# Performance work log

Measured on AMD Instinct MI355X. Metric: run time of the kernel, lower is better.

## Reference

```python
import jax, jax.numpy as jnp
import numpy as np

DIM = 1024

def setup_inputs() -> dict:
    key = jax.random.key(0)
    k1, k2, k3, k4 = jax.random.split(key, 4)
    B, L, D = 32, 2048, DIM
    x = jax.random.normal(k1, (B, D), dtype=jnp.float32)
    context = jax.random.normal(k2, (B, L, D), dtype=jnp.float32)
    # linear_concatWa: Linear(2*dim, dim, bias=False) -> weight [dim, 2*dim]
    Wa = jax.random.normal(k3, (D, 2 * D), dtype=jnp.float32) * (1.0 / np.sqrt(2 * D))
    # linear_concatVa: Linear(dim, 1, bias=False) -> weight [1, dim]
    Va = jax.random.normal(k4, (1, D), dtype=jnp.float32) * (1.0 / np.sqrt(D))
    return {"x": x, "context": context, "Wa": Wa, "Va": Va}


def reference(x, context, Wa, Va):
    # concat-mode additive (Bahdanau) attention.
    # Wa @ cat(ht, hs) == ht @ Wa[:, :D].T + hs @ Wa[:, D:].T  (avoids materializing concat)
    D = x.shape[-1]
    Wa_t, Wa_s = Wa[:, :D], Wa[:, D:]              # each [D, D]
    ht_proj = jnp.einsum('bd,kd->bk', x, Wa_t)     # [B, D]
    hs_proj = jnp.einsum('bld,kd->blk', context, Wa_s)  # [B, L, D]
    hidden = jnp.tanh(ht_proj[:, None, :] + hs_proj)    # [B, L, D]
    scores = jnp.einsum('blk,ok->bl', hidden, Va)       # [B, L]  (Va: [1, D])
    attn = jax.nn.softmax(scores, axis=-1)               # [B, L]
    weighted = jnp.einsum('bl,bld->bd', attn, context)   # [B, D]
    return weighted, attn
```

## Files before the change

kernel.cpp:

```cpp
#include <hip/hip_runtime.h>
#include <hip/hip_bf16.h>
#include <cstdint>
#include <cstddef>

#define DIM 1024
#define B_SZ 32
#define L_SZ 2048

#define BM 128
#define BN 128

#define CVT_BLOCKS 8192
#define HT_BLOCKS  512
#define WA_BLOCKS  512

typedef __attribute__((ext_vector_type(8))) short bf16x8;
typedef __attribute__((ext_vector_type(4))) float floatx4;

static __device__ __forceinline__ unsigned cvt2_bf16_rne(float a, float b) {
    unsigned ua = __builtin_bit_cast(unsigned, a);
    unsigned ub = __builtin_bit_cast(unsigned, b);
    ua = (ua + 0x7FFFu + ((ua >> 16) & 1u)) >> 16;
    ub = (ub + 0x7FFFu + ((ub >> 16) & 1u)) >> 16;
    return ua | (ub << 16);
}

static __device__ __forceinline__ float bf2f(unsigned u16) {
    return __builtin_bit_cast(float, u16 << 16);
}

static __device__ __forceinline__ float tanh_fast(float x) {
    float e = __expf(2.0f * x);
    return 1.0f - 2.0f * __builtin_amdgcn_rcpf(e + 1.0f);
}

static __device__ __forceinline__ void gld_lds16(const void* g, void* lds) {
    __builtin_amdgcn_global_load_lds(
        (const __attribute__((address_space(1))) unsigned int*)g,
        (__attribute__((address_space(3))) unsigned int*)lds,
        16, 0, 0);
}

static __device__ __forceinline__ bf16x8 dsr128(unsigned addr) {
    bf16x8 r;
    asm volatile("ds_read_b128 %0, %1" : "=v"(r) : "v"(addr));
    return r;
}

#define VMCNT(n)  asm volatile("s_waitcnt vmcnt(" #n ")" ::: "memory")
#define SBAR()    asm volatile("s_barrier" ::: "memory")
#define WAITK()   do { asm volatile("s_waitcnt lgkmcnt(0)" ::: "memory"); \
                       __builtin_amdgcn_sched_barrier(0); } while (0)

__global__ __launch_bounds__(256) void pre_kernel(
    const float* __restrict__ x, const float* __restrict__ ctx,
    const float* __restrict__ Wa,
    unsigned short* __restrict__ ctxB, unsigned short* __restrict__ WaB,
    float* __restrict__ ht, float* __restrict__ scores,
    float* __restrict__ weighted)
{
    const int bid = blockIdx.x, t = threadIdx.x;

    if (bid < CVT_BLOCKS) {
        const long n8 = (long)B_SZ * L_SZ * DIM / 8;
        const long stride = (long)CVT_BLOCKS * 256;
        for (long i = (long)bid * 256 + t; i < n8; i += stride) {
            const float4 a = ((const float4*)ctx)[i * 2];
            const float4 b = ((const float4*)ctx)[i * 2 + 1];
            uint4 o;
            o.x = cvt2_bf16_rne(a.x, a.y);
            o.y = cvt2_bf16_rne(a.z, a.w);
            o.z = cvt2_bf16_rne(b.x, b.y);
            o.w = cvt2_bf16_rne(b.z, b.w);
            ((uint4*)ctxB)[i] = o;
        }
    } else if (bid < CVT_BLOCKS + HT_BLOCKS) {
        const int lb = bid - CVT_BLOCKS;
        const int gi = lb * 256 + t;
        if (gi < B_SZ * L_SZ) scores[gi] = 0.f;
        const int b = lb >> 4, kb = lb & 15;
        __shared__ float xs[DIM];
        for (int i = t; i < DIM; i += 256) xs[i] = x[b * DIM + i];
        __syncthreads();
        const int wave = t >> 6, lane = t & 63;
        const float4* xs4 = (const float4*)xs;
        for (int kk = 0; kk < 16; ++kk) {
            const int k = kb * 64 + wave * 16 + kk;
            const float4* wr = (const float4*)(Wa + (size_t)k * (2 * DIM));
            float s = 0.f;
            #pragma unroll
            for (int d = 0; d < DIM / 4; d += 64) {
                const float4 w4 = wr[d + lane];
                const float4 x4 = xs4[d + lane];
                s += w4.x * x4.x + w4.y * x4.y + w4.z * x4.z + w4.w * x4.w;
            }
            #pragma unroll
            for (int off = 32; off > 0; off >>= 1) s += __shfl_xor(s, off);
            if (lane == 0) ht[b * DIM + k] = s;
        }
    } else {
        const int lb = bid - CVT_BLOCKS - HT_BLOCKS;
        const int i = lb * 256 + t;
        if (i < B_SZ * DIM) weighted[i] = 0.f;
        const int k = i >> 7, dc = i & 127;
        const float* s = Wa + (size_t)k * (2 * DIM) + DIM + dc * 8;
        const float4 a = ((const float4*)s)[0];
        const float4 b4 = ((const float4*)s)[1];
        uint4 o;
        o.x = cvt2_bf16_rne(a.x, a.y);
        o.y = cvt2_bf16_rne(a.z, a.w);
        o.z = cvt2_bf16_rne(b4.x, b4.y);
        o.w = cvt2_bf16_rne(b4.z, b4.w);
        ((uint4*)(WaB + (size_t)k * DIM + dc * 8))[0] = o;
    }
}

static __device__ __forceinline__ void lda4(
    unsigned base, int wr, int l15, int quad, bf16x8 (&af)[4][2])
{
    #pragma unroll
    for (int i = 0; i < 4; ++i) {
        const int r = wr + i * 16 + l15;
        #pragma unroll
        for (int kb = 0; kb < 2; ++kb) {
            const int c = (kb * 4 + quad) ^ (r & 7);
            af[i][kb] = dsr128(base + (unsigned)(r * 128 + c * 16));
        }
    }
}

static __device__ __forceinline__ void ldb2(
    unsigned base, int wc, int l15, int quad, bf16x8 (&bv)[2][2])
{
    #pragma unroll
    for (int j = 0; j < 2; ++j) {
        const int r = wc + j * 16 + l15;
        #pragma unroll
        for (int kb = 0; kb < 2; ++kb) {
            const int c = (kb * 4 + quad) ^ (r & 7);
            bv[j][kb] = dsr128(base + (unsigned)(r * 128 + c * 16));
        }
    }
}

static __device__ __forceinline__ void mma16(
    floatx4 (&acc)[4][2], const bf16x8 (&af)[4][2], const bf16x8 (&bv)[2][2])
{
    __builtin_amdgcn_s_setprio(1);
    #pragma unroll
    for (int kb = 0; kb < 2; ++kb)
        #pragma unroll
        for (int i = 0; i < 4; ++i)
            #pragma unroll
            for (int j = 0; j < 2; ++j)
                acc[i][j] = __builtin_amdgcn_mfma_f32_16x16x32_bf16(
                    af[i][kb], bv[j][kb], acc[i][j], 0, 0, 0);
    __builtin_amdgcn_s_setprio(0);
}

static __device__ __forceinline__ void stage_half(
    const unsigned short* __restrict__ g, unsigned short* lds, int t, int wave)
{
    #pragma unroll
    for (int q = 0; q < 2; ++q) {
        const int ch = q * 512 + t;
        const int lr = ch >> 3;
        const int lc = (ch & 7) ^ (lr & 7);
        gld_lds16(g + (size_t)lr * DIM + lc * 8, lds + (q * 512 + wave * 64) * 8);
    }
}

__global__ __launch_bounds__(512, 2) void gemm_score_8ph(
    const unsigned short* __restrict__ A, const unsigned short* __restrict__ Bm,
    const float* __restrict__ Va, const float* __restrict__ ht,
    float* __restrict__ scores)
{
    __shared__ __align__(16) unsigned short As[2][2][128 * 64];
    __shared__ __align__(16) unsigned short Bs[2][2][128 * 64];

    const int bid = blockIdx.x;
    const int logical = (bid & 7) * 128 + (bid >> 3);
    const int m0 = (logical >> 2) * 256;
    const int n0 = (logical & 3) * 256;

    const int t = threadIdx.x;
    const int lane = t & 63, wave = t >> 6;
    const int l15 = lane & 15, quad = lane >> 4;
    const int wr = (wave >> 2) * 64;
    const int wc = (wave & 3) * 32;

    const unsigned short* Ag = A + (size_t)m0 * DIM;
    const unsigned short* Bg = Bm + (size_t)n0 * DIM;

    const unsigned aB = (unsigned)(unsigned long long)&As[0][0][0];
    const unsigned bB = (unsigned)(unsigned long long)&Bs[0][0][0];
    const unsigned a00 = aB, a01 = aB + 16384, a10 = aB + 32768, a11 = aB + 49152;
    const unsigned b00 = bB, b01 = bB + 16384, b10 = bB + 32768, b11 = bB + 49152;

    floatx4 acc[4][4][2];
    #pragma unroll
    for (int q = 0; q < 4; ++q)
        #pragma unroll
        for (int i = 0; i < 4; ++i)
            #pragma unroll
            for (int j = 0; j < 2; ++j) acc[q][i][j] = (floatx4)0.f;

    bf16x8 af[4][2], bvA[2][2], bvB[2][2];

    stage_half(Ag, &As[0][0][0], t, wave);
    stage_half(Bg, &Bs[0][0][0], t, wave);
    stage_half(Bg + (size_t)128 * DIM, &Bs[0][1][0], t, wave);
    stage_half(Ag + (size_t)128 * DIM, &As[0][1][0], t, wave);
    stage_half(Ag + 64, &As[1][0][0], t, wave);
    stage_half(Bg + (size_t)128 * DIM + 64, &Bs[1][1][0], t, wave);
    VMCNT(4);
    SBAR();

    for (int it = 0; it < 8; ++it) {
        const int k1 = (2 * it + 1) * 64;
        const int k2 = (2 * it + 2) * 64;
        const int k3 = (2 * it + 3) * 64;
        const bool more = (it < 7);

        lda4(a00, wr, l15, quad, af);
        ldb2(b00, wc, l15, quad, bvA);
        stage_half(Bg + k1, &Bs[1][0][0], t, wave);
        SBAR();
        WAITK();
        mma16(acc[0], af, bvA);
        SBAR();

        ldb2(b01, wc, l15, quad, bvB);
        stage_half(Ag + (size_t)128 * DIM + k1, &As[1][1][0], t, wave);
        if (more) stage_half(Bg + k2, &Bs[0][0][0], t, wave);
        SBAR();
        WAITK();
        mma16(acc[1], af, bvB);
        SBAR();

        lda4(a01, wr, l15, quad, af);
        SBAR();
        WAITK();
        mma16(acc[3], af, bvB);
        SBAR();

        if (more) { stage_half(Ag + k2, &As[0][0][0], t, wave); VMCNT(2); }
        else      { VMCNT(0); }
        SBAR();
        mma16(acc[2], af, bvA);
        SBAR();

        lda4(a10, wr, l15, quad, af);
        ldb2(b10, wc, l15, quad, bvA);
        if (more) stage_half(Bg + (size_t)128 * DIM + k2, &Bs[0][1][0], t, wave);
        SBAR();
        WAITK();
        mma16(acc[0], af, bvA);
        SBAR();

        ldb2(b11, wc, l15, quad, bvB);
        if (more) stage_half(Ag + (size_t)128 * DIM + k2, &As[0][1][0], t, wave);
        SBAR();
        WAITK();
        mma16(acc[1], af, bvB);
        SBAR();

        lda4(a11, wr, l15, quad, af);
        if (more) stage_half(Ag + k3, &As[1][0][0], t, wave);
        SBAR();
        WAITK();
        mma16(acc[3], af, bvB);
        SBAR();

        if (more) {
            stage_half(Bg + (size_t)128 * DIM + k3, &Bs[1][1][0], t, wave);
            VMCNT(4);
        }
        SBAR();
        mma16(acc[2], af, bvA);
        SBAR();
    }

    const int bb = m0 >> 11;
    float htv[2][2], vav[2][2];
    #pragma unroll
    for (int qc = 0; qc < 2; ++qc)
        #pragma unroll
        for (int j = 0; j < 2; ++j) {
            const int ng = n0 + qc * 128 + wc + j * 16 + l15;
            htv[qc][j] = ht[bb * DIM + ng];
            vav[qc][j] = Va[ng];
        }
    #pragma unroll
    for (int qr = 0; qr < 2; ++qr)
        #pragma unroll
        for (int i = 0; i < 4; ++i)
            #pragma unroll
            for (int r = 0; r < 4; ++r) {
                float s = 0.f;
                #pragma unroll
                for (int qc = 0; qc < 2; ++qc)
                    #pragma unroll
                    for (int j = 0; j < 2; ++j)
                        s += tanh_fast(acc[qr * 2 + qc][i][j][r] + htv[qc][j]) * vav[qc][j];
                s += __shfl_xor(s, 8);
                s += __shfl_xor(s, 4);
                s += __shfl_xor(s, 2);
                s += __shfl_xor(s, 1);
                if (l15 == 0)
                    atomicAdd(&scores[m0 + qr * 128 + wr + i * 16 + quad * 4 + r], s);
            }
}

__global__ __launch_bounds__(256) void post_kernel(
    const float* __restrict__ scores, const unsigned short* __restrict__ ctxB,
    float* __restrict__ attn, float* __restrict__ weighted)
{
    const int b = blockIdx.x, slice = blockIdx.y, t = threadIdx.x;
    const float* sc = scores + b * L_SZ;
    __shared__ float red[256];
    __shared__ float att[128];

    float m = -1e30f;
    for (int l = t; l < L_SZ; l += 256) m = fmaxf(m, sc[l]);
    red[t] = m; __syncthreads();
    for (int s = 128; s > 0; s >>= 1) { if (t < s) red[t] = fmaxf(red[t], red[t + s]); __syncthreads(); }
    m = red[0]; __syncthreads();
    float sum = 0.f;
    for (int l = t; l < L_SZ; l += 256) sum += __expf(sc[l] - m);
    red[t] = sum; __syncthreads();
    for (int s = 128; s > 0; s >>= 1) { if (t < s) red[t] += red[t + s]; __syncthreads(); }
    const float inv = 1.0f / red[0];

    const int l0 = slice * 128;
    if (t < 128) {
        const float av = __expf(sc[l0 + t] - m) * inv;
        att[t] = av;
        attn[b * L_SZ + l0 + t] = av;
    }
    __syncthreads();

    const unsigned short* cb = ctxB + ((size_t)b * L_SZ + l0) * DIM + t * 4;
    float a0 = 0.f, a1 = 0.f, a2 = 0.f, a3 = 0.f;
    for (int l = 0; l < 128; ++l) {
        const float a = att[l];
        const uint2 v = *(const uint2*)(cb + (size_t)l * DIM);
        a0 += a * bf2f(v.x & 0xFFFFu);
        a1 += a * bf2f(v.x >> 16);
        a2 += a * bf2f(v.y & 0xFFFFu);
        a3 += a * bf2f(v.y >> 16);
    }
    float* o = weighted + b * DIM + t * 4;
    atomicAdd(o + 0, a0);
    atomicAdd(o + 1, a1);
    atomicAdd(o + 2, a2);
    atomicAdd(o + 3, a3);
}

#define LDS_STRIDE 40
__global__ __launch_bounds__(256) void ht_kernel_fb(const float* __restrict__ x,
                                                    const float* __restrict__ Wa,
                                                    float* __restrict__ ht,
                                                    float* __restrict__ scores,
                                                    float* __restrict__ weighted) {
    const int b = blockIdx.x, kb = blockIdx.y, t = threadIdx.x;
    const int gidx = (b * 16 + kb) * 256 + t;
    if (gidx < B_SZ * L_SZ) scores[gidx] = 0.f;
    if (gidx < B_SZ * DIM) weighted[gidx] = 0.f;
    __shared__ float xs[DIM];
    for (int i = t; i < DIM; i += 256) xs[i] = x[b * DIM + i];
    __syncthreads();
    const int wave = t >> 6, lane = t & 63;
    for (int kk = 0; kk < 16; ++kk) {
        const int k = kb * 64 + wave * 16 + kk;
        const float* wr = Wa + (size_t)k * (2 * DIM);
        float s = 0.f;
        #pragma unroll
        for (int d = 0; d < DIM; d += 64) s += xs[d + lane] * wr[d + lane];
        #pragma unroll
        for (int off = 32; off > 0; off >>= 1) s += __shfl_xor(s, off);
        if (lane == 0) ht[b * DIM + k] = s;
    }
}

__global__ __launch_bounds__(256, 2) void gemm_score_kernel(
    const float* __restrict__ ctx, const float* __restrict__ Wa,
    const float* __restrict__ Va, const float* __restrict__ ht,
    float* __restrict__ scores)
{
    __shared__ unsigned short As[BM * LDS_STRIDE];
    __shared__ unsigned short Bs[BN * LDS_STRIDE];
    const int t = threadIdx.x;
    const int n0 = blockIdx.x * BN;
    const int m0 = blockIdx.y * BM;
    const int lane = t & 63, wave = t >> 6;
    const int l15 = lane & 15, quad = lane >> 4;
    const int wm = (wave >> 1) * 64, wn = (wave & 1) * 64;
    const int srow = t >> 3;
    const int scol = (t & 7) * 4;
    const float* aBase = ctx + (size_t)(m0 + srow) * DIM + scol;
    const float* bBase = Wa + (size_t)(n0 + srow) * (2 * DIM) + DIM + scol;

    floatx4 acc[4][4];
    #pragma unroll
    for (int i = 0; i < 4; ++i)
        #pragma unroll
        for (int j = 0; j < 4; ++j) acc[i][j] = (floatx4)0.f;

    for (int k0 = 0; k0 < DIM; k0 += 32) {
        __syncthreads();
        #pragma unroll
        for (int r = 0; r < 4; ++r) {
            const float4 va = *(const float4*)(aBase + (size_t)(r * 32) * DIM + k0);
            const float4 vb = *(const float4*)(bBase + (size_t)(r * 32) * (2 * DIM) + k0);
            *(uint2*)&As[(srow + r * 32) * LDS_STRIDE + scol] =
                make_uint2(cvt2_bf16_rne(va.x, va.y), cvt2_bf16_rne(va.z, va.w));
            *(uint2*)&Bs[(srow + r * 32) * LDS_STRIDE + scol] =
                make_uint2(cvt2_bf16_rne(vb.x, vb.y), cvt2_bf16_rne(vb.z, vb.w));
        }
        __syncthreads();
        bf16x8 af[4], bfr[4];
        #pragma unroll
        for (int i = 0; i < 4; ++i)
            af[i] = *(const bf16x8*)&As[(wm + i * 16 + l15) * LDS_STRIDE + quad * 8];
        #pragma unroll
        for (int j = 0; j < 4; ++j)
            bfr[j] = *(const bf16x8*)&Bs[(wn + j * 16 + l15) * LDS_STRIDE + quad * 8];
        #pragma unroll
        for (int i = 0; i < 4; ++i)
            #pragma unroll
            for (int j = 0; j < 4; ++j)
                acc[i][j] = __builtin_amdgcn_mfma_f32_16x16x32_bf16(af[i], bfr[j], acc[i][j], 0, 0, 0);
    }
    const int bb = m0 >> 11;
    float htv[4], vav[4];
    #pragma unroll
    for (int j = 0; j < 4; ++j) {
        const int ng = n0 + wn + j * 16 + l15;
        htv[j] = ht[bb * DIM + ng];
        vav[j] = Va[ng];
    }
    #pragma unroll
    for (int i = 0; i < 4; ++i) {
        #pragma unroll
        for (int r = 0; r < 4; ++r) {
            float s = 0.f;
            #pragma unroll
            for (int j = 0; j < 4; ++j)
                s += tanh_fast(acc[i][j][r] + htv[j]) * vav[j];
            s += __shfl_xor(s, 8);
            s += __shfl_xor(s, 4);
            s += __shfl_xor(s, 2);
            s += __shfl_xor(s, 1);
            if (l15 == 0)
                atomicAdd(&scores[m0 + wm + i * 16 + quad * 4 + r], s);
        }
    }
}

__global__ __launch_bounds__(256) void post_kernel_fb(
    const float* __restrict__ scores, const float* __restrict__ ctx,
    float* __restrict__ attn, float* __restrict__ weighted)
{
    const int b = blockIdx.x, slice = blockIdx.y, t = threadIdx.x;
    const float* sc = scores + b * L_SZ;
    __shared__ float red[256];
    __shared__ float att[128];
    float m = -1e30f;
    for (int l = t; l < L_SZ; l += 256) m = fmaxf(m, sc[l]);
    red[t] = m; __syncthreads();
    for (int s = 128; s > 0; s >>= 1) { if (t < s) red[t] = fmaxf(red[t], red[t + s]); __syncthreads(); }
    m = red[0]; __syncthreads();
    float sum = 0.f;
    for (int l = t; l < L_SZ; l += 256) sum += __expf(sc[l] - m);
    red[t] = sum; __syncthreads();
    for (int s = 128; s > 0; s >>= 1) { if (t < s) red[t] += red[t + s]; __syncthreads(); }
    const float inv = 1.0f / red[0];
    const int l0 = slice * 128;
    if (t < 128) {
        const float av = __expf(sc[l0 + t] - m) * inv;
        att[t] = av;
        attn[b * L_SZ + l0 + t] = av;
    }
    __syncthreads();
    const float* cb = ctx + ((size_t)b * L_SZ + l0) * DIM + t * 4;
    float4 w = make_float4(0.f, 0.f, 0.f, 0.f);
    for (int l = 0; l < 128; ++l) {
        const float a = att[l];
        const float4 c = *(const float4*)(cb + (size_t)l * DIM);
        w.x += a * c.x; w.y += a * c.y; w.z += a * c.z; w.w += a * c.w;
    }
    float* o = weighted + b * DIM + t * 4;
    atomicAdd(o + 0, w.x);
    atomicAdd(o + 1, w.y);
    atomicAdd(o + 2, w.z);
    atomicAdd(o + 3, w.w);
}

extern "C" void kernel_launch(void* const* d_in, const int* in_sizes, int n_in,
                              void* d_out, int out_size, void* d_ws, size_t ws_size,
                              hipStream_t stream) {
    const float* x   = (const float*)d_in[0];
    const float* ctx = (const float*)d_in[1];
    const float* Wa  = (const float*)d_in[2];
    const float* Va  = (const float*)d_in[3];

    float* out      = (float*)d_out;
    float* weighted = out;
    float* attn     = out + B_SZ * DIM;

    float* scores = (float*)d_ws;
    float* ht     = scores + B_SZ * L_SZ;

    const size_t base = (size_t)(B_SZ * L_SZ + B_SZ * DIM) * sizeof(float);
    const size_t need = base + (size_t)DIM * DIM * 2
                      + (size_t)B_SZ * L_SZ * DIM * 2;

    if (ws_size >= need) {
        unsigned short* WaB  = (unsigned short*)((char*)d_ws + base);
        unsigned short* ctxB = WaB + (size_t)DIM * DIM;
        pre_kernel<<<CVT_BLOCKS + HT_BLOCKS + WA_BLOCKS, 256, 0, stream>>>(
            x, ctx, Wa, ctxB, WaB, ht, scores, weighted);
        gemm_score_8ph<<<(B_SZ * L_SZ / 256) * (DIM / 256), 512, 0, stream>>>(
            ctxB, WaB, Va, ht, scores);
        post_kernel<<<dim3(B_SZ, 16), 256, 0, stream>>>(scores, ctxB, attn, weighted);
    } else {
        ht_kernel_fb<<<dim3(B_SZ, 16), 256, 0, stream>>>(x, Wa, ht, scores, weighted);
        gemm_score_kernel<<<dim3(DIM / BN, (B_SZ * L_SZ) / BM), 256, 0, stream>>>(
            ctx, Wa, Va, ht, scores);
        post_kernel_fb<<<dim3(B_SZ, 16), 256, 0, stream>>>(scores, ctx, attn, weighted);
    }
}
```

Baseline: 617.1 us.

## Rework context conversion loop, split softmax stats kernel, relax GEMM occupancy bound

The fp32-to-bf16 context conversion now uses a fixed four-iteration unrolled loop with coalesced float4 loads and uint2 stores, replacing the grid-stride loop. The softmax is split into a separate per-batch stats kernel, so the 16 post blocks per batch no longer each redo the max and sum reductions; they read precomputed attn instead, and their accumulation loop is unrolled. The GEMM launch bound drops from 2 to 1 blocks per CU, which allows more registers per thread but may lower occupancy. The extra kernel launch adds a little fixed overhead.

After: 617.2 us. No clear change (+0.0%).

```diff
diff --git a/kernel.cpp b/kernel.cpp
--- a/kernel.cpp
+++ b/kernel.cpp
@@ -62,17 +62,15 @@
     const int bid = blockIdx.x, t = threadIdx.x;
 
     if (bid < CVT_BLOCKS) {
-        const long n8 = (long)B_SZ * L_SZ * DIM / 8;
-        const long stride = (long)CVT_BLOCKS * 256;
-        for (long i = (long)bid * 256 + t; i < n8; i += stride) {
-            const float4 a = ((const float4*)ctx)[i * 2];
-            const float4 b = ((const float4*)ctx)[i * 2 + 1];
-            uint4 o;
-            o.x = cvt2_bf16_rne(a.x, a.y);
-            o.y = cvt2_bf16_rne(a.z, a.w);
-            o.z = cvt2_bf16_rne(b.x, b.y);
-            o.w = cvt2_bf16_rne(b.z, b.w);
-            ((uint4*)ctxB)[i] = o;
+        const float4* c4 = (const float4*)ctx;
+        uint2* o2 = (uint2*)ctxB;
+        #pragma unroll
+        for (int it = 0; it < 4; ++it) {
+            const long g = ((long)it * CVT_BLOCKS + bid) * 512;
+            const float4 a = c4[g + t];
+            const float4 b = c4[g + 256 + t];
+            o2[g + t]       = make_uint2(cvt2_bf16_rne(a.x, a.y), cvt2_bf16_rne(a.z, a.w));
+            o2[g + 256 + t] = make_uint2(cvt2_bf16_rne(b.x, b.y), cvt2_bf16_rne(b.z, b.w));
         }
     } else if (bid < CVT_BLOCKS + HT_BLOCKS) {
         const int lb = bid - CVT_BLOCKS;
@@ -170,7 +168,7 @@
     }
 }
 
-__global__ __launch_bounds__(512, 2) void gemm_score_8ph(
+__global__ __launch_bounds__(512, 1) void gemm_score_8ph(
     const unsigned short* __restrict__ A, const unsigned short* __restrict__ Bm,
     const float* __restrict__ Va, const float* __restrict__ ht,
     float* __restrict__ scores)
@@ -312,14 +310,12 @@
             }
 }
 
-__global__ __launch_bounds__(256) void post_kernel(
-    const float* __restrict__ scores, const unsigned short* __restrict__ ctxB,
-    float* __restrict__ attn, float* __restrict__ weighted)
-{
-    const int b = blockIdx.x, slice = blockIdx.y, t = threadIdx.x;
+__global__ __launch_bounds__(256) void stats_kernel(
+    const float* __restrict__ scores, float* __restrict__ attn)
+{
+    const int b = blockIdx.x, t = threadIdx.x;
     const float* sc = scores + b * L_SZ;
     __shared__ float red[256];
-    __shared__ float att[128];
 
     float m = -1e30f;
     for (int l = t; l < L_SZ; l += 256) m = fmaxf(m, sc[l]);
@@ -332,16 +328,23 @@
     for (int s = 128; s > 0; s >>= 1) { if (t < s) red[t] += red[t + s]; __syncthreads(); }
     const float inv = 1.0f / red[0];
 
+    for (int l = t; l < L_SZ; l += 256)
+        attn[b * L_SZ + l] = __expf(sc[l] - m) * inv;
+}
+
+__global__ __launch_bounds__(256) void post_kernel(
+    const float* __restrict__ attn, const unsigned short* __restrict__ ctxB,
+    float* __restrict__ weighted)
+{
+    const int b = blockIdx.x, slice = blockIdx.y, t = threadIdx.x;
+    __shared__ float att[128];
     const int l0 = slice * 128;
-    if (t < 128) {
-        const float av = __expf(sc[l0 + t] - m) * inv;
-        att[t] = av;
-        attn[b * L_SZ + l0 + t] = av;
-    }
+    if (t < 128) att[t] = attn[b * L_SZ + l0 + t];
     __syncthreads();
 
     const unsigned short* cb = ctxB + ((size_t)b * L_SZ + l0) * DIM + t * 4;
     float a0 = 0.f, a1 = 0.f, a2 = 0.f, a3 = 0.f;
+    #pragma unroll 4
     for (int l = 0; l < 128; ++l) {
         const float a = att[l];
         const uint2 v = *(const uint2*)(cb + (size_t)l * DIM);
@@ -523,7 +526,8 @@
             x, ctx, Wa, ctxB, WaB, ht, scores, weighted);
         gemm_score_8ph<<<(B_SZ * L_SZ / 256) * (DIM / 256), 512, 0, stream>>>(
             ctxB, WaB, Va, ht, scores);
-        post_kernel<<<dim3(B_SZ, 16), 256, 0, stream>>>(scores, ctxB, attn, weighted);
+        stats_kernel<<<B_SZ, 256, 0, stream>>>(scores, attn);
+        post_kernel<<<dim3(B_SZ, 16), 256, 0, stream>>>(attn, ctxB, weighted);
     } else {
         ht_kernel_fb<<<dim3(B_SZ, 16), 256, 0, stream>>>(x, Wa, ht, scores, weighted);
         gemm_score_kernel<<<dim3(DIM / BN, (B_SZ * L_SZ) / BM), 256, 0, stream>>>(
```
